# Kernel optimization log

Measured on AMD Instinct MI355X. Metric: run time of the kernel, lower is better.

The kernel has to match this reference:

```python
import jax, jax.numpy as jnp
import numpy as np

B, L, D_MODEL, H = 2, 2048, 1024, 16
D_K = D_MODEL // H


def entmax15(z):
    """Exact 1.5-entmax along last axis (Peters et al. 2019, sort-based)."""
    z = z - jnp.max(z, axis=-1, keepdims=True)
    z = z / 2.0
    K = z.shape[-1]
    z_sorted = -jnp.sort(-z, axis=-1)  # descending
    kk = jnp.arange(1, K + 1, dtype=z.dtype)
    cs = jnp.cumsum(z_sorted, axis=-1)
    cs2 = jnp.cumsum(z_sorted * z_sorted, axis=-1)
    mean = cs / kk
    ss = cs2 - cs * mean                 # k * (E[z^2] - E[z]^2)
    delta = (1.0 - ss) / kk
    tau = mean - jnp.sqrt(jnp.clip(delta, 0.0))
    support = jnp.sum((tau <= z_sorted).astype(jnp.int32), axis=-1, keepdims=True)
    tau_star = jnp.take_along_axis(tau, support - 1, axis=-1)
    p = jnp.clip(z - tau_star, 0.0)
    return p * p


def setup_inputs() -> dict:
    key = jax.random.key(0)
    ks = jax.random.split(key, 8)
    s = 1.0 / np.sqrt(D_MODEL)
    return {
        "q": jax.random.normal(ks[0], (B, L, D_MODEL), jnp.float32),
        "k": jax.random.normal(ks[1], (B, L, D_MODEL), jnp.float32),
        "v": jax.random.normal(ks[2], (B, L, D_MODEL), jnp.float32),
        "mask": jnp.ones((B, L, L), jnp.int32),
        "w_q": jax.random.normal(ks[3], (D_MODEL, D_MODEL), jnp.float32) * s,
        "w_k": jax.random.normal(ks[4], (D_MODEL, D_MODEL), jnp.float32) * s,
        "w_v": jax.random.normal(ks[5], (D_MODEL, D_MODEL), jnp.float32) * s,
        "w_o": jax.random.normal(ks[6], (D_MODEL, D_MODEL), jnp.float32) * s,
    }


def reference(q, k, v, mask, w_q, w_k, w_v, w_o):
    b, l, _ = q.shape
    # torch Linear (no bias): y = x @ W^T
    def proj(x, w):
        return jnp.einsum('bld,ed->ble', x, w).reshape(b, l, H, D_K).transpose(0, 2, 1, 3)
    Q, K, V = proj(q, w_q), proj(k, w_k), proj(v, w_v)  # [B,H,L,d_k]
    scores = jnp.einsum('bhqd,bhkd->bhqk', Q, K) / np.sqrt(D_K)
    scores = jnp.where(mask[:, None, :, :] == 0, jnp.finfo(scores.dtype).min, scores)
    probs = entmax15(scores)
    out = jnp.einsum('bhqk,bhkd->bhqd', probs, V)
    out = out.transpose(0, 2, 1, 3).reshape(b, l, D_MODEL)
    return jnp.einsum('bld,ed->ble', out, w_o)
```

## Files before the change

kernel.cpp:

```cpp
#include <hip/hip_runtime.h>


typedef _Float16 f16;
typedef __attribute__((ext_vector_type(8))) _Float16 f16x8;
typedef __attribute__((ext_vector_type(4))) _Float16 f16x4;
typedef __attribute__((ext_vector_type(2))) _Float16 f16x2;
typedef __attribute__((ext_vector_type(4))) float f32x4;
typedef unsigned int u32;

static __device__ __forceinline__ f16x2 max2(f16x2 a, f16x2 b) {
    return __builtin_elementwise_max(a, b);
}

static __device__ __forceinline__ f16x2 shfl2(f16x2 v, int off) {
    union { f16x2 h; int i; } u;
    u.h = v;
    u.i = __shfl_xor(u.i, off);
    return u.h;
}

static __device__ __forceinline__ f16x2 pkrtz(float a, float b) {
    union { __fp16 __attribute__((ext_vector_type(2))) p; f16x2 h; } u;
    u.p = __builtin_amdgcn_cvt_pkrtz(a, b);
    return u.h;
}

__global__ __launch_bounds__(256)
void pack_mask(const int* __restrict__ mask, u32* __restrict__ bits)
{
    int idx = blockIdx.x * 256 + threadIdx.x;
    const int4* p = (const int4*)&mask[(size_t)idx * 32];
    u32 v = 0;
#pragma unroll
    for (int i = 0; i < 8; i++) {
        int4 m = p[i];
        if (m.x != 0) v |= 1u << (i * 4 + 0);
        if (m.y != 0) v |= 1u << (i * 4 + 1);
        if (m.z != 0) v |= 1u << (i * 4 + 2);
        if (m.w != 0) v |= 1u << (i * 4 + 3);
    }
    const int wd = idx & 63;
    const int q = (idx >> 6) & 2047;
    const int b = idx >> 17;
    bits[(((size_t)(b * 128 + (q >> 4)) * 8 + (wd >> 3)) << 7) + ((q & 15) << 3) + (wd & 7)] = v;
}

__global__ __launch_bounds__(512)
void gemm_qkv(const float* __restrict__ Aq, const float* __restrict__ Ak,
              const float* __restrict__ Av, const float* __restrict__ W0,
              const float* __restrict__ W1, const float* __restrict__ W2,
              f16* __restrict__ Qp, f16* __restrict__ Kp, f16* __restrict__ Vp)
{
    __shared__ __align__(16) f16 As[128 * 40];
    __shared__ __align__(16) f16 Bs[128 * 40];

    const int tid = threadIdx.x;
    const int wsel = blockIdx.y >> 3;
    const float* A  = wsel == 0 ? Aq : (wsel == 1 ? Ak : Av);
    const float* Wp = wsel == 0 ? W0 : (wsel == 1 ? W1 : W2);
    const int mBase = blockIdx.x * 128;
    const int nBase = (blockIdx.y & 7) * 128;

    const int lane = tid & 63, w = tid >> 6;
    const int g = lane >> 4, c = lane & 15;
    const int wm = w >> 1, wn = w & 1;

    const int sr = tid >> 2;
    const int sq = tid & 3;

    f32x4 acc[2][4];
    const f32x4 vzero = {0.f, 0.f, 0.f, 0.f};
#pragma unroll
    for (int i = 0; i < 2; i++)
#pragma unroll
        for (int j = 0; j < 4; j++) acc[i][j] = vzero;

    for (int k0 = 0; k0 < 1024; k0 += 32) {
        __syncthreads();
        {
            const float4* p = (const float4*)&A[(size_t)(mBase + sr) * 1024 + k0 + sq * 8];
            float4 x0 = p[0], x1 = p[1];
            f16x8 av;
            av[0] = (f16)x0.x; av[1] = (f16)x0.y; av[2] = (f16)x0.z; av[3] = (f16)x0.w;
            av[4] = (f16)x1.x; av[5] = (f16)x1.y; av[6] = (f16)x1.z; av[7] = (f16)x1.w;
            *(f16x8*)&As[sr * 40 + sq * 8] = av;

            const float4* pw = (const float4*)&Wp[(size_t)(nBase + sr) * 1024 + k0 + sq * 8];
            float4 w0 = pw[0], w1 = pw[1];
            f16x8 bv;
            bv[0] = (f16)w0.x; bv[1] = (f16)w0.y; bv[2] = (f16)w0.z; bv[3] = (f16)w0.w;
            bv[4] = (f16)w1.x; bv[5] = (f16)w1.y; bv[6] = (f16)w1.z; bv[7] = (f16)w1.w;
            *(f16x8*)&Bs[sr * 40 + sq * 8] = bv;
        }
        __syncthreads();

        f16x8 af[2], bf[4];
#pragma unroll
        for (int mt = 0; mt < 2; mt++)
            af[mt] = *(const f16x8*)&As[(wm * 32 + mt * 16 + c) * 40 + g * 8];
#pragma unroll
        for (int nt = 0; nt < 4; nt++)
            bf[nt] = *(const f16x8*)&Bs[(wn * 64 + nt * 16 + c) * 40 + g * 8];
#pragma unroll
        for (int mt = 0; mt < 2; mt++)
#pragma unroll
            for (int nt = 0; nt < 4; nt++)
                acc[mt][nt] = __builtin_amdgcn_mfma_f32_16x16x32_f16(af[mt], bf[nt], acc[mt][nt], 0, 0, 0);
    }

#pragma unroll
    for (int mt = 0; mt < 2; mt++)
#pragma unroll
        for (int nt = 0; nt < 4; nt++) {
            int row0 = mBase + wm * 32 + mt * 16 + g * 4;
            int col = nBase + wn * 64 + nt * 16 + c;
            if (wsel == 2) {
                int b = row0 >> 11, l0 = row0 & 2047;
                int h = col >> 6, dk = col & 63;
                int bh = b * 16 + h;
                int t = l0 >> 4, gv = (l0 & 15) >> 2;
                int nd = dk >> 4, c16 = dk & 15;
                f16x4 pv;
#pragma unroll
                for (int r = 0; r < 4; r++) pv[r] = (f16)acc[mt][nt][r];
                *(f16x4*)&Vp[(size_t)(bh * 128 + t) * 1024 + nd * 256 + c16 * 16 + gv * 4] = pv;
            } else {
                f16* Cp = wsel == 0 ? Qp : Kp;
                const float scale = wsel == 0 ? 0.0625f : 1.0f;
#pragma unroll
                for (int r = 0; r < 4; r++) {
                    int row = row0 + r;
                    float v = acc[mt][nt][r] * scale;
                    int b = row >> 11, l = row & 2047;
                    int h = col >> 6, dk = col & 63;
                    int bh = b * 16 + h;
                    int t = l >> 4, ck = l & 15;
                    int half = dk >> 5, gk = (dk >> 3) & 3, e = dk & 7;
                    Cp[((size_t)(bh * 128 + t) * 2 + half) * 512 + ck * 32 + gk * 8 + e] = (f16)v;
                }
            }
        }
}

__global__ __launch_bounds__(512)
void gemm_out(const f16* __restrict__ Ap, const float* __restrict__ Wp,
              float* __restrict__ Cp)
{
    __shared__ __align__(16) f16 As[128 * 40];
    __shared__ __align__(16) f16 Bs[128 * 40];

    const int tid = threadIdx.x;
    const int mBase = blockIdx.x * 128;
    const int nBase = blockIdx.y * 128;

    const int lane = tid & 63, w = tid >> 6;
    const int g = lane >> 4, c = lane & 15;
    const int wm = w >> 1, wn = w & 1;

    const int sr = tid >> 2;
    const int sq = tid & 3;

    f32x4 acc[2][4];
    const f32x4 vzero = {0.f, 0.f, 0.f, 0.f};
#pragma unroll
    for (int i = 0; i < 2; i++)
#pragma unroll
        for (int j = 0; j < 4; j++) acc[i][j] = vzero;

    for (int k0 = 0; k0 < 1024; k0 += 32) {
        __syncthreads();
        {
            *(f16x8*)&As[sr * 40 + sq * 8] =
                *(const f16x8*)&Ap[(size_t)(mBase + sr) * 1024 + k0 + sq * 8];

            const float4* pw = (const float4*)&Wp[(size_t)(nBase + sr) * 1024 + k0 + sq * 8];
            float4 w0 = pw[0], w1 = pw[1];
            f16x8 bv;
            bv[0] = (f16)w0.x; bv[1] = (f16)w0.y; bv[2] = (f16)w0.z; bv[3] = (f16)w0.w;
            bv[4] = (f16)w1.x; bv[5] = (f16)w1.y; bv[6] = (f16)w1.z; bv[7] = (f16)w1.w;
            *(f16x8*)&Bs[sr * 40 + sq * 8] = bv;
        }
        __syncthreads();

        f16x8 af[2], bf[4];
#pragma unroll
        for (int mt = 0; mt < 2; mt++)
            af[mt] = *(const f16x8*)&As[(wm * 32 + mt * 16 + c) * 40 + g * 8];
#pragma unroll
        for (int nt = 0; nt < 4; nt++)
            bf[nt] = *(const f16x8*)&Bs[(wn * 64 + nt * 16 + c) * 40 + g * 8];
#pragma unroll
        for (int mt = 0; mt < 2; mt++)
#pragma unroll
            for (int nt = 0; nt < 4; nt++)
                acc[mt][nt] = __builtin_amdgcn_mfma_f32_16x16x32_f16(af[mt], bf[nt], acc[mt][nt], 0, 0, 0);
    }

#pragma unroll
    for (int mt = 0; mt < 2; mt++)
#pragma unroll
        for (int nt = 0; nt < 4; nt++) {
            int row0 = mBase + wm * 32 + mt * 16 + g * 4;
            int col = nBase + wn * 64 + nt * 16 + c;
#pragma unroll
            for (int r = 0; r < 4; r++)
                Cp[(size_t)(row0 + r) * 1024 + col] = acc[mt][nt][r];
        }
}

__global__ __launch_bounds__(512, 2)
void attn_entmax(const f16* __restrict__ Qp, const f16* __restrict__ Kp,
                 const f16* __restrict__ Vp, const u32* __restrict__ Mp,
                 f16* __restrict__ AO)
{
    constexpr int CAP = 512;
    constexpr int BSTR = 514;
    __shared__ __align__(16) char LB[8 * 32 * 72 * 2];
    __shared__ int cntS[32];
    __shared__ float redM[8][32];
    __shared__ float redN[2][8][32][2];
    __shared__ float tau2s[32], zmaxs[32], taus[32];

    f16* bucket = (f16*)LB;
    f16* Ored = (f16*)LB;

    const int tid = threadIdx.x;
    const int w = tid >> 6, lane = tid & 63;
    const int g = lane >> 4, c = lane & 15;

    const int bid = blockIdx.x;
    const int q6 = bid >> 3;
    const int bh = (bid & 7) * 4 + (q6 >> 6);
    const int qt = q6 & 63;
    const int qb = qt * 32;
    const int b = bh >> 4, h = bh & 15;

    if (tid < 32) cntS[tid] = 0;

    const f16* qbaseA = &Qp[(size_t)(bh * 128 + 2 * qt) * 1024 + c * 32 + g * 8];
    f16x8 bqA0 = *(const f16x8*)qbaseA;
    f16x8 bqA1 = *(const f16x8*)(qbaseA + 512);
    f16x8 bqB0 = *(const f16x8*)(qbaseA + 1024);
    f16x8 bqB1 = *(const f16x8*)(qbaseA + 1536);

    const u32* mbaseA = &Mp[(((size_t)(b * 128 + 2 * qt) * 8 + w) << 7) + (c << 3)];
    uint4 mA0 = *(const uint4*)mbaseA;
    uint4 mA1 = *(const uint4*)(mbaseA + 4);
    uint4 mB0 = *(const uint4*)(mbaseA + 128);
    uint4 mB1 = *(const uint4*)(mbaseA + 132);
    u32 mbA[8] = {mA0.x, mA0.y, mA0.z, mA0.w, mA1.x, mA1.y, mA1.z, mA1.w};
    u32 mbB[8] = {mB0.x, mB0.y, mB0.z, mB0.w, mB1.x, mB1.y, mB1.z, mB1.w};

    f16x2 hSA[32], hSB[32];
    f16x2 rmaxA; rmaxA.x = (f16)(-30000.f); rmaxA.y = (f16)(-30000.f);
    f16x2 rmaxB = rmaxA;
    const f32x4 vz = {0.f, 0.f, 0.f, 0.f};
    const f16* kbaseP = &Kp[(size_t)(bh * 128 + w * 16) * 1024 + c * 32 + g * 8];
#pragma unroll
    for (int t = 0; t < 16; t++) {
        const f16* kp = kbaseP + (size_t)t * 1024;
        f16x8 ka0 = *(const f16x8*)kp;
        f16x8 ka1 = *(const f16x8*)(kp + 512);
        f32x4 zA = __builtin_amdgcn_mfma_f32_16x16x32_f16(ka0, bqA0, vz, 0, 0, 0);
        zA = __builtin_amdgcn_mfma_f32_16x16x32_f16(ka1, bqA1, zA, 0, 0, 0);
        f32x4 zB = __builtin_amdgcn_mfma_f32_16x16x32_f16(ka0, bqB0, vz, 0, 0, 0);
        zB = __builtin_amdgcn_mfma_f32_16x16x32_f16(ka1, bqB1, zB, 0, 0, 0);
        u32 mwA = mbA[t >> 1], mwB = mbB[t >> 1];
        if (__builtin_expect(mwA != 0xFFFFFFFFu, 0)) {
            u32 b4 = mwA >> ((t & 1) * 16 + g * 4);
#pragma unroll
            for (int r = 0; r < 4; r++)
                if (!((b4 >> r) & 1)) zA[r] = -30000.f;
        }
        if (__builtin_expect(mwB != 0xFFFFFFFFu, 0)) {
            u32 b4 = mwB >> ((t & 1) * 16 + g * 4);
#pragma unroll
            for (int r = 0; r < 4; r++)
                if (!((b4 >> r) & 1)) zB[r] = -30000.f;
        }
        f16x2 a0 = pkrtz(zA[0], zA[1]), a1 = pkrtz(zA[2], zA[3]);
        f16x2 b0 = pkrtz(zB[0], zB[1]), b1 = pkrtz(zB[2], zB[3]);
        hSA[2 * t] = a0; hSA[2 * t + 1] = a1;
        hSB[2 * t] = b0; hSB[2 * t + 1] = b1;
        rmaxA = max2(rmaxA, max2(a0, a1));
        rmaxB = max2(rmaxB, max2(b0, b1));
    }

    float zxA = fmaxf((float)rmaxA.x, (float)rmaxA.y);
    float zxB = fmaxf((float)rmaxB.x, (float)rmaxB.y);
    zxA = fmaxf(zxA, __shfl_xor(zxA, 16)); zxA = fmaxf(zxA, __shfl_xor(zxA, 32));
    zxB = fmaxf(zxB, __shfl_xor(zxB, 16)); zxB = fmaxf(zxB, __shfl_xor(zxB, 32));
    if (lane < 16) { redM[w][c] = zxA; redM[w][16 + c] = zxB; }
    __syncthreads();
    float zmaxA = -3e38f, zmaxB = -3e38f;
#pragma unroll
    for (int ww = 0; ww < 8; ww++) {
        zmaxA = fmaxf(zmaxA, redM[ww][c]);
        zmaxB = fmaxf(zmaxB, redM[ww][16 + c]);
    }

    f16x2 zero2; zero2.x = (f16)0.f; zero2.y = (f16)0.f;
    float tauA = zmaxA - 1.0f, tauB = zmaxB - 1.0f;
    int buf = 0;
#pragma unroll 1
    for (int it = 0; it < 2; ++it) {
        f16 tnA = (f16)tauA, tnB = (f16)tauB;
        f16x2 tvA; tvA.x = tnA; tvA.y = tnA;
        f16x2 tvB; tvB.x = tnB; tvB.y = tnB;
        f16x2 s1A = zero2, s2A = zero2, s1B = zero2, s2B = zero2;
#pragma unroll
        for (int i = 0; i < 32; i++) {
            f16x2 dA = max2(hSA[i] - tvA, zero2);
            f16x2 dB = max2(hSB[i] - tvB, zero2);
            s1A = s1A + dA; s2A = s2A + dA * dA;
            s1B = s1B + dB; s2B = s2B + dB * dB;
        }
        s1A = s1A + shfl2(s1A, 16); s2A = s2A + shfl2(s2A, 16);
        s1A = s1A + shfl2(s1A, 32); s2A = s2A + shfl2(s2A, 32);
        s1B = s1B + shfl2(s1B, 16); s2B = s2B + shfl2(s2B, 16);
        s1B = s1B + shfl2(s1B, 32); s2B = s2B + shfl2(s2B, 32);
        float a1 = (float)s1A.x + (float)s1A.y;
        float f1 = (float)s2A.x + (float)s2A.y;
        float a2 = (float)s1B.x + (float)s1B.y;
        float f2 = (float)s2B.x + (float)s2B.y;
        if (lane < 16) {
            redN[buf][w][c][0] = a1; redN[buf][w][c][1] = f1;
            redN[buf][w][16 + c][0] = a2; redN[buf][w][16 + c][1] = f2;
        }
        __syncthreads();
        float aA = 0.f, fA = 0.f, aB = 0.f, fB = 0.f;
#pragma unroll
        for (int ww = 0; ww < 8; ww++) {
            float2 vA = *(const float2*)&redN[buf][ww][c][0];
            float2 vB = *(const float2*)&redN[buf][ww][16 + c][0];
            aA += vA.x; fA += vA.y;
            aB += vB.x; fB += vB.y;
        }
        if (aA > 1e-9f) tauA = fminf(tauA + (fA - 1.0f) / (2.0f * aA), zmaxA - 1e-3f);
        if (aB > 1e-9f) tauB = fminf(tauB + (fB - 1.0f) / (2.0f * aB), zmaxB - 1e-3f);
        buf ^= 1;
    }
    if (w == 0 && lane < 16) {
        tau2s[c] = tauA; tau2s[16 + c] = tauB;
        zmaxs[c] = zmaxA; zmaxs[16 + c] = zmaxB;
    }

    const f16 thrA = (f16)(tauA - 0.02f);
    const f16 thrB = (f16)(tauB - 0.02f);
    f16x2 thrA2; thrA2.x = thrA; thrA2.y = thrA;
    f16x2 thrB2; thrB2.x = thrB; thrB2.y = thrB;
#pragma unroll
    for (int i = 0; i < 32; i++) {
        union { f16x2 h; u32 u; } dA, dB;
        dA.h = hSA[i] - thrA2;
        dB.h = hSB[i] - thrB2;
        u32 posA = ~dA.u & 0x80008000u;
        u32 posB = ~dB.u & 0x80008000u;
        if (__builtin_expect(posA != 0, 0)) {
            if (hSA[i].x > thrA) { int id = atomicAdd(&cntS[c], 1); if (id < CAP) bucket[c * BSTR + id] = hSA[i].x; }
            if (hSA[i].y > thrA) { int id = atomicAdd(&cntS[c], 1); if (id < CAP) bucket[c * BSTR + id] = hSA[i].y; }
        }
        if (__builtin_expect(posB != 0, 0)) {
            if (hSB[i].x > thrB) { int id = atomicAdd(&cntS[16 + c], 1); if (id < CAP) bucket[(16 + c) * BSTR + id] = hSB[i].x; }
            if (hSB[i].y > thrB) { int id = atomicAdd(&cntS[16 + c], 1); if (id < CAP) bucket[(16 + c) * BSTR + id] = hSB[i].y; }
        }
    }
    __syncthreads();

    {
        const int qi = 4 * w + (lane >> 4);
        const int sl = lane & 15;
        const int cnt = min(cntS[qi], CAP);
        const int ns = (cnt + 15) >> 4;
        float tq = tau2s[qi];
        const float zq = zmaxs[qi];
#pragma unroll 1
        for (int it = 0; it < 4; ++it) {
            float s1 = 0.f, s2 = 0.f;
#pragma unroll 1
            for (int s = 0; s < ns; s++) {
                int i = sl + 16 * s;
                float v = (i < cnt) ? (float)bucket[qi * BSTR + i] : -1e30f;
                float d = fmaxf(v - tq, 0.f);
                s1 += d; s2 = fmaf(d, d, s2);
            }
#pragma unroll
            for (int off = 1; off <= 8; off <<= 1) {
                s1 += __shfl_xor(s1, off);
                s2 += __shfl_xor(s2, off);
            }
            if (s1 > 1e-12f) tq = fminf(tq + (s2 - 1.0f) / (2.0f * s1), zq - 1e-3f);
        }
#pragma unroll 1
        for (int rf = 0; rf < 3; ++rf) {
            float kc = 0.f, s1 = 0.f, s2 = 0.f;
#pragma unroll 1
            for (int s = 0; s < ns; s++) {
                int i = sl + 16 * s;
                float v = (i < cnt) ? (float)bucket[qi * BSTR + i] : -1e30f;
                float d = v - tq;
                if (d > 0.f) { kc += 1.f; s1 += d; s2 = fmaf(d, d, s2); }
            }
#pragma unroll
            for (int off = 1; off <= 8; off <<= 1) {
                kc += __shfl_xor(kc, off);
                s1 += __shfl_xor(s1, off);
                s2 += __shfl_xor(s2, off);
            }
            float K_ = fmaxf(kc, 1.0f);
            float disc = fmaxf(s1 * s1 - K_ * (s2 - 1.0f), 0.f);
            tq += (s1 - sqrtf(disc)) / K_;
        }
        if (sl == 0) taus[qi] = tq;
    }
    __syncthreads();

    const f16 tcA = (f16)taus[c];
    const f16 tcB = (f16)taus[16 + c];
    f16x2 tvA2; tvA2.x = tcA; tvA2.y = tcA;
    f16x2 tvB2; tvB2.x = tcB; tvB2.y = tcB;
    f32x4 O0[4], O1[4];
#pragma unroll
    for (int nd = 0; nd < 4; nd++) { O0[nd] = vz; O1[nd] = vz; }
    const f16* vbase = &Vp[(size_t)(bh * 128 + w * 16) * 1024 + c * 16 + g * 4];
#pragma unroll
    for (int t = 0; t < 16; t++) {
        f16x2 daA = max2(hSA[2 * t] - tvA2, zero2);
        f16x2 dbA = max2(hSA[2 * t + 1] - tvA2, zero2);
        f16x2 daB = max2(hSB[2 * t] - tvB2, zero2);
        f16x2 dbB = max2(hSB[2 * t + 1] - tvB2, zero2);
        daA = daA * daA; dbA = dbA * dbA;
        daB = daB * daB; dbB = dbB * dbB;
        union { f16x4 v4; f16x2 h2[2]; } puA, puB;
        puA.h2[0] = daA; puA.h2[1] = dbA;
        puB.h2[0] = daB; puB.h2[1] = dbB;
        const f16* vp = vbase + (size_t)t * 1024;
#pragma unroll
        for (int nd = 0; nd < 4; nd++) {
            f16x4 va = *(const f16x4*)(vp + nd * 256);
            O0[nd] = __builtin_amdgcn_mfma_f32_16x16x16f16(va, puA.v4, O0[nd], 0, 0, 0);
            O1[nd] = __builtin_amdgcn_mfma_f32_16x16x16f16(va, puB.v4, O1[nd], 0, 0, 0);
        }
    }

#pragma unroll
    for (int nd = 0; nd < 4; nd++) {
        union { f16x4 v4; f16x2 h2[2]; } p0, p1;
        p0.h2[0] = pkrtz(O0[nd][0], O0[nd][1]);
        p0.h2[1] = pkrtz(O0[nd][2], O0[nd][3]);
        p1.h2[0] = pkrtz(O1[nd][0], O1[nd][1]);
        p1.h2[1] = pkrtz(O1[nd][2], O1[nd][3]);
        *(f16x4*)&Ored[(w * 32 + c) * 72 + nd * 16 + g * 4] = p0.v4;
        *(f16x4*)&Ored[(w * 32 + 16 + c) * 72 + nd * 16 + g * 4] = p1.v4;
    }
    __syncthreads();

    const int qr = tid >> 4;
    const int d0 = (tid & 15) * 4;
    float4 accv = {0.f, 0.f, 0.f, 0.f};
#pragma unroll
    for (int ww = 0; ww < 8; ww++) {
        f16x4 v = *(const f16x4*)&Ored[(ww * 32 + qr) * 72 + d0];
        accv.x += (float)v[0]; accv.y += (float)v[1];
        accv.z += (float)v[2]; accv.w += (float)v[3];
    }
    f16x4 pk;
    pk[0] = (f16)accv.x; pk[1] = (f16)accv.y; pk[2] = (f16)accv.z; pk[3] = (f16)accv.w;
    *(f16x4*)&AO[(size_t)(b * 2048 + qb + qr) * 1024 + h * 64 + d0] = pk;
}

extern "C" void kernel_launch(void* const* d_in, const int* in_sizes, int n_in,
                              void* d_out, int out_size, void* d_ws, size_t ws_size,
                              hipStream_t stream)
{
    const float* q  = (const float*)d_in[0];
    const float* k  = (const float*)d_in[1];
    const float* v  = (const float*)d_in[2];
    const int* mask = (const int*)d_in[3];
    const float* wq = (const float*)d_in[4];
    const float* wk = (const float*)d_in[5];
    const float* wv = (const float*)d_in[6];
    const float* wo = (const float*)d_in[7];

    char* ws = (char*)d_ws;
    const size_t SZ = 8388608ull;
    f16* Qb  = (f16*)(ws);
    f16* Kb  = (f16*)(ws + SZ);
    f16* Vb  = (f16*)(ws + 2 * SZ);
    f16* AOb = (f16*)(ws + 3 * SZ);
    u32* Mb  = (u32*)(ws + 4 * SZ);

    pack_mask<<<1024, 256, 0, stream>>>(mask, Mb);
    gemm_qkv<<<dim3(32, 24), 512, 0, stream>>>(q, k, v, wq, wk, wv, Qb, Kb, Vb);
    attn_entmax<<<2048, 512, 0, stream>>>(Qb, Kb, Vb, Mb, AOb);
    gemm_out<<<dim3(32, 8), 512, 0, stream>>>(AOb, wo, (float*)d_out);
}
```

Before: 337.8 us.

## Split entmax attention into tau-finding kernel and score-recomputing PV kernel

```diff
diff --git a/kernel.cpp b/kernel.cpp
--- a/kernel.cpp
+++ b/kernel.cpp
@@ -209,20 +209,16 @@
 }
 
 __global__ __launch_bounds__(512, 2)
-void attn_entmax(const f16* __restrict__ Qp, const f16* __restrict__ Kp,
-                 const f16* __restrict__ Vp, const u32* __restrict__ Mp,
-                 f16* __restrict__ AO)
+void attn_tau(const f16* __restrict__ Qp, const f16* __restrict__ Kp,
+              const u32* __restrict__ Mp, float* __restrict__ TauG)
 {
     constexpr int CAP = 512;
     constexpr int BSTR = 514;
-    __shared__ __align__(16) char LB[8 * 32 * 72 * 2];
+    __shared__ __align__(16) f16 bucket[32 * BSTR];
     __shared__ int cntS[32];
     __shared__ float redM[8][32];
     __shared__ float redN[2][8][32][2];
-    __shared__ float tau2s[32], zmaxs[32], taus[32];
-
-    f16* bucket = (f16*)LB;
-    f16* Ored = (f16*)LB;
+    __shared__ float tau2s[32], zmaxs[32];
 
     const int tid = threadIdx.x;
     const int w = tid >> 6, lane = tid & 63;
@@ -233,7 +229,7 @@
     const int bh = (bid & 7) * 4 + (q6 >> 6);
     const int qt = q6 & 63;
     const int qb = qt * 32;
-    const int b = bh >> 4, h = bh & 15;
+    const int b = bh >> 4;
 
     if (tid < 32) cntS[tid] = 0;
 
@@ -411,29 +407,83 @@
             float disc = fmaxf(s1 * s1 - K_ * (s2 - 1.0f), 0.f);
             tq += (s1 - sqrtf(disc)) / K_;
         }
-        if (sl == 0) taus[qi] = tq;
-    }
-    __syncthreads();
-
-    const f16 tcA = (f16)taus[c];
-    const f16 tcB = (f16)taus[16 + c];
-    f16x2 tvA2; tvA2.x = tcA; tvA2.y = tcA;
-    f16x2 tvB2; tvB2.x = tcB; tvB2.y = tcB;
+        if (sl == 0) TauG[(size_t)bh * 2048 + qb + qi] = tq;
+    }
+}
+
+__global__ __launch_bounds__(512, 2)
+void attn_pv(const f16* __restrict__ Qp, const f16* __restrict__ Kp,
+             const f16* __restrict__ Vp, const u32* __restrict__ Mp,
+             const float* __restrict__ TauG, f16* __restrict__ AO)
+{
+    __shared__ __align__(16) f16 Ored[8 * 32 * 72];
+
+    const int tid = threadIdx.x;
+    const int w = tid >> 6, lane = tid & 63;
+    const int g = lane >> 4, c = lane & 15;
+
+    const int bid = blockIdx.x;
+    const int q6 = bid >> 3;
+    const int bh = (bid & 7) * 4 + (q6 >> 6);
+    const int qt = q6 & 63;
+    const int qb = qt * 32;
+    const int b = bh >> 4, h = bh & 15;
+
+    const f16* qbaseA = &Qp[(size_t)(bh * 128 + 2 * qt) * 1024 + c * 32 + g * 8];
+    f16x8 bqA0 = *(const f16x8*)qbaseA;
+    f16x8 bqA1 = *(const f16x8*)(qbaseA + 512);
+    f16x8 bqB0 = *(const f16x8*)(qbaseA + 1024);
+    f16x8 bqB1 = *(const f16x8*)(qbaseA + 1536);
+
+    const float tauA = TauG[(size_t)bh * 2048 + qb + c];
+    const float tauB = TauG[(size_t)bh * 2048 + qb + 16 + c];
+
+    const u32* mbaseA = &Mp[(((size_t)(b * 128 + 2 * qt) * 8 + w) << 7) + (c << 3)];
+    uint4 mA0 = *(const uint4*)mbaseA;
+    uint4 mA1 = *(const uint4*)(mbaseA + 4);
+    uint4 mB0 = *(const uint4*)(mbaseA + 128);
+    uint4 mB1 = *(const uint4*)(mbaseA + 132);
+    u32 mbA[8] = {mA0.x, mA0.y, mA0.z, mA0.w, mA1.x, mA1.y, mA1.z, mA1.w};
+    u32 mbB[8] = {mB0.x, mB0.y, mB0.z, mB0.w, mB1.x, mB1.y, mB1.z, mB1.w};
+
+    const f32x4 vz = {0.f, 0.f, 0.f, 0.f};
     f32x4 O0[4], O1[4];
 #pragma unroll
     for (int nd = 0; nd < 4; nd++) { O0[nd] = vz; O1[nd] = vz; }
+    const f16* kbaseP = &Kp[(size_t)(bh * 128 + w * 16) * 1024 + c * 32 + g * 8];
     const f16* vbase = &Vp[(size_t)(bh * 128 + w * 16) * 1024 + c * 16 + g * 4];
+
 #pragma unroll
     for (int t = 0; t < 16; t++) {
-        f16x2 daA = max2(hSA[2 * t] - tvA2, zero2);
-        f16x2 dbA = max2(hSA[2 * t + 1] - tvA2, zero2);
-        f16x2 daB = max2(hSB[2 * t] - tvB2, zero2);
-        f16x2 dbB = max2(hSB[2 * t + 1] - tvB2, zero2);
-        daA = daA * daA; dbA = dbA * dbA;
-        daB = daB * daB; dbB = dbB * dbB;
+        const f16* kp = kbaseP + (size_t)t * 1024;
+        f16x8 ka0 = *(const f16x8*)kp;
+        f16x8 ka1 = *(const f16x8*)(kp + 512);
+        f32x4 zA = __builtin_amdgcn_mfma_f32_16x16x32_f16(ka0, bqA0, vz, 0, 0, 0);
+        zA = __builtin_amdgcn_mfma_f32_16x16x32_f16(ka1, bqA1, zA, 0, 0, 0);
+        f32x4 zB = __builtin_amdgcn_mfma_f32_16x16x32_f16(ka0, bqB0, vz, 0, 0, 0);
+        zB = __builtin_amdgcn_mfma_f32_16x16x32_f16(ka1, bqB1, zB, 0, 0, 0);
+        u32 mwA = mbA[t >> 1], mwB = mbB[t >> 1];
+        if (__builtin_expect(mwA != 0xFFFFFFFFu, 0)) {
+            u32 b4 = mwA >> ((t & 1) * 16 + g * 4);
+#pragma unroll
+            for (int r = 0; r < 4; r++)
+                if (!((b4 >> r) & 1)) zA[r] = -30000.f;
+        }
+        if (__builtin_expect(mwB != 0xFFFFFFFFu, 0)) {
+            u32 b4 = mwB >> ((t & 1) * 16 + g * 4);
+#pragma unroll
+            for (int r = 0; r < 4; r++)
+                if (!((b4 >> r) & 1)) zB[r] = -30000.f;
+        }
+        float dA0 = fmaxf(zA[0] - tauA, 0.f), dA1 = fmaxf(zA[1] - tauA, 0.f);
+        float dA2 = fmaxf(zA[2] - tauA, 0.f), dA3 = fmaxf(zA[3] - tauA, 0.f);
+        float dB0 = fmaxf(zB[0] - tauB, 0.f), dB1 = fmaxf(zB[1] - tauB, 0.f);
+        float dB2 = fmaxf(zB[2] - tauB, 0.f), dB3 = fmaxf(zB[3] - tauB, 0.f);
         union { f16x4 v4; f16x2 h2[2]; } puA, puB;
-        puA.h2[0] = daA; puA.h2[1] = dbA;
-        puB.h2[0] = daB; puB.h2[1] = dbB;
+        puA.h2[0] = pkrtz(dA0 * dA0, dA1 * dA1);
+        puA.h2[1] = pkrtz(dA2 * dA2, dA3 * dA3);
+        puB.h2[0] = pkrtz(dB0 * dB0, dB1 * dB1);
+        puB.h2[1] = pkrtz(dB2 * dB2, dB3 * dB3);
         const f16* vp = vbase + (size_t)t * 1024;
 #pragma unroll
         for (int nd = 0; nd < 4; nd++) {
@@ -489,9 +539,11 @@
     f16* Vb  = (f16*)(ws + 2 * SZ);
     f16* AOb = (f16*)(ws + 3 * SZ);
     u32* Mb  = (u32*)(ws + 4 * SZ);
+    float* TauG = (float*)(ws + 4 * SZ + 1048576ull);
 
     pack_mask<<<1024, 256, 0, stream>>>(mask, Mb);
     gemm_qkv<<<dim3(32, 24), 512, 0, stream>>>(q, k, v, wq, wk, wv, Qb, Kb, Vb);
-    attn_entmax<<<2048, 512, 0, stream>>>(Qb, Kb, Vb, Mb, AOb);
+    attn_tau<<<2048, 512, 0, stream>>>(Qb, Kb, Mb, TauG);
+    attn_pv<<<2048, 512, 0, stream>>>(Qb, Kb, Vb, Mb, TauG, AOb);
     gemm_out<<<dim3(32, 8), 512, 0, stream>>>(AOb, wo, (float*)d_out);
 }
```

Result: slower. 354.6 us (+5.0%).
